# Kernel tuning notes

Measured on AMD Instinct MI355X. Metric: run time of the kernel, lower is better.

## Reference

```python
import jax, jax.numpy as jnp
import numpy as np

EPS = 1e-7
ROUTINGS = 3


def squash(s, axis=-1):
    # norm over `axis`; faithful to torch: (|s|^2/(1+|s|^2)) * (s/(|s|+eps))
    norm = jnp.linalg.norm(s, axis=axis, keepdims=True)
    sq = norm * norm
    return (sq / (1.0 + sq)) * (s / (norm + EPS))


def conv2d(x, w, b, stride):
    y = jax.lax.conv_general_dilated(
        x, w, window_strides=(stride, stride), padding='VALID',
        dimension_numbers=('NCHW', 'OIHW', 'NCHW'))
    return y + b[None, :, None, None]


def setup_inputs() -> dict:
    key = jax.random.key(0)
    ks = jax.random.split(key, 12)
    B = 256
    return {
        'x': jax.random.normal(ks[0], (B, 1, 28, 28), dtype=jnp.float32),
        'conv1_w': 0.05 * jax.random.normal(ks[1], (256, 1, 9, 9), dtype=jnp.float32),
        'conv1_b': jnp.zeros((256,), jnp.float32),
        'conv2_w': 0.02 * jax.random.normal(ks[2], (256, 256, 9, 9), dtype=jnp.float32),
        'conv2_b': jnp.zeros((256,), jnp.float32),
        'W_caps': 0.01 * jax.random.normal(ks[3], (10, 1152, 16, 8), dtype=jnp.float32),
        'dec_w1': 0.05 * jax.random.normal(ks[4], (160, 512), dtype=jnp.float32),
        'dec_b1': jnp.zeros((512,), jnp.float32),
        'dec_w2': 0.04 * jax.random.normal(ks[5], (512, 1024), dtype=jnp.float32),
        'dec_b2': jnp.zeros((1024,), jnp.float32),
        'dec_w3': 0.03 * jax.random.normal(ks[6], (1024, 784), dtype=jnp.float32),
        'dec_b3': jnp.zeros((784,), jnp.float32),
    }


def reference(x, conv1_w, conv1_b, conv2_w, conv2_b, W_caps,
              dec_w1, dec_b1, dec_w2, dec_b2, dec_w3, dec_b3):
    B = x.shape[0]
    # conv1: [B,1,28,28] -> [B,256,20,20]
    h = conv2d(x, conv1_w, conv1_b, stride=1)
    # primary capsules: conv -> [B,256,6,6]
    h = conv2d(h, conv2_w, conv2_b, stride=2)
    # faithful to original: squash over the LAST spatial axis (dim=-1)
    h = squash(h, axis=-1)
    u = h.reshape(B, -1, 8)  # [B,1152,8]

    # u_hat[b,o,i,d] = W_caps[o,i,d,e] @ u[b,i,e]  -> [B,10,1152,16]
    u_hat = jnp.einsum('oide,bie->boid', W_caps, u)
    u_hat_det = jax.lax.stop_gradient(u_hat)

    b_logits = jnp.zeros((B, 10, 1152), u_hat.dtype)
    for it in range(ROUTINGS):
        c = jax.nn.softmax(b_logits, axis=1)  # over output capsules
        if it == ROUTINGS - 1:
            v = squash(jnp.sum(c[:, :, :, None] * u_hat, axis=-2, keepdims=True))
        else:
            v = squash(jnp.sum(c[:, :, :, None] * u_hat_det, axis=-2, keepdims=True))
            b_logits = b_logits + jnp.sum(v * u_hat_det, axis=-1)
    v = jnp.squeeze(v, axis=-2)  # [B,10,16]

    length = jnp.linalg.norm(v, axis=-1)  # [B,10]
    # y defaults to one-hot of argmax(length), constant w.r.t. grads
    y = jax.lax.stop_gradient(
        jax.nn.one_hot(jnp.argmax(length, axis=1), 10, dtype=v.dtype))
    masked = (v * y[:, :, None]).reshape(B, -1)  # [B,160]
    h1 = jax.nn.relu(masked @ dec_w1 + dec_b1)
    h2 = jax.nn.relu(h1 @ dec_w2 + dec_b2)
    reconstruction = jax.nn.sigmoid(h2 @ dec_w3 + dec_b3)  # [B,784]
    return length, reconstruction
```

## Files before the change

### kernel.cpp

```cpp
#include <hip/hip_runtime.h>
#include <cstdint>
#include <cstddef>

typedef __bf16 bf16x8 __attribute__((ext_vector_type(8)));
typedef float  floatx4 __attribute__((ext_vector_type(4)));
typedef float  floatx2 __attribute__((ext_vector_type(2)));
typedef float  floatx16 __attribute__((ext_vector_type(16)));
typedef int    intx4v __attribute__((ext_vector_type(4)));
typedef int    intx8 __attribute__((ext_vector_type(8)));
typedef unsigned short ushort8 __attribute__((ext_vector_type(8)));
typedef unsigned short ushort4v __attribute__((ext_vector_type(4)));

__device__ __forceinline__ float bflo(unsigned int u) {
    union { unsigned int u32; float f; } x; x.u32 = u << 16; return x.f;
}
__device__ __forceinline__ float bfhi(unsigned int u) {
    union { unsigned int u32; float f; } x; x.u32 = u & 0xffff0000u; return x.f;
}
__device__ __forceinline__ unsigned short f2bf(float f) {
    union { float f; unsigned int u; } x; x.f = f;
    unsigned int u = x.u;
    unsigned int r = (u + 0x7fffu + ((u >> 16) & 1u)) >> 16;
    return (unsigned short)r;
}
__device__ __forceinline__ unsigned char f2fp8(float f) {
    unsigned int pk = __builtin_amdgcn_cvt_pk_fp8_f32(f, f, 0, false);
    return (unsigned char)(pk & 0xff);
}
__device__ __forceinline__ void fp8x4_dec(unsigned int u, float* f) {
    floatx2 lo = __builtin_amdgcn_cvt_pk_f32_fp8(u, false);
    floatx2 hi = __builtin_amdgcn_cvt_pk_f32_fp8(u, true);
    f[0] = lo[0]; f[1] = lo[1]; f[2] = hi[0]; f[3] = hi[1];
}

#define GLOBAL_U32 const __attribute__((address_space(1))) unsigned int*
#define LDS_U32 __attribute__((address_space(3))) unsigned int*
__device__ __forceinline__ void async_cp16(const void* g, void* l) {
    __builtin_amdgcn_global_load_lds((GLOBAL_U32)g, (LDS_U32)l, 16, 0, 0);
}

#define UHAT_SCALE 64.0f
#define UHAT_INV   (1.0f / 64.0f)
#define W2_SCALE   16.0f
#define W2_INV     (1.0f / 16.0f)

__global__ __launch_bounds__(256) void prep_k(const float* __restrict__ x,
                                              const float* __restrict__ w1c,
                                              const float* __restrict__ b1c,
                                              const float* __restrict__ w2,
                                              unsigned char* __restrict__ h1t8,
                                              unsigned char* __restrict__ w2t8,
                                              float* __restrict__ S012) {
    const int blk = blockIdx.x, t = threadIdx.x;
    if (t < 120) S012[blk * 120 + t] = 0.f;
    __shared__ float shm[10368];
    if (blk < 512) {
        const int b = blk >> 1, hh = blk & 1;
        const int oh0 = hh * 10;
        for (int idx = t; idx < 504; idx += 256) shm[idx] = x[b * 784 + oh0 * 28 + idx];
        __syncthreads();
        const float* wr = w1c + t * 81;
        const float bv = b1c[t];
        for (int ohl = 0; ohl < 10; ++ohl) {
            float acc[20];
#pragma unroll
            for (int ow = 0; ow < 20; ++ow) acc[ow] = bv;
#pragma unroll
            for (int kh = 0; kh < 9; ++kh) {
                float xr[28];
                const float* xrow = &shm[(ohl + kh) * 28];
#pragma unroll
                for (int q = 0; q < 7; ++q) *(float4*)&xr[q * 4] = *(const float4*)&xrow[q * 4];
#pragma unroll
                for (int kw = 0; kw < 9; ++kw) {
                    const float wv = wr[kh * 9 + kw];
#pragma unroll
                    for (int ow = 0; ow < 20; ++ow) acc[ow] = fmaf(xr[ow + kw], wv, acc[ow]);
                }
            }
            unsigned char* orow = h1t8 + (size_t)((b * 20 + oh0 + ohl) * 20) * 256 + t;
#pragma unroll
            for (int ow = 0; ow < 20; ++ow) orow[ow * 256] = f2fp8(acc[ow]);
        }
    } else {
        const int id = blk - 512;
        const int oc = id >> 1, half = id & 1;
        const float* src = w2 + (size_t)oc * 20736 + half * 128 * 81;
        for (int idx = t; idx < 10368; idx += 256) shm[idx] = src[idx];
        __syncthreads();
        unsigned char* dst = w2t8 + (size_t)oc * 20736 + half * 128;
        for (int idx = t; idx < 10368; idx += 256) {
            const int tap = idx >> 7, icl = idx & 127;
            dst[tap * 256 + icl] = f2fp8(shm[icl * 81 + tap] * W2_SCALE);
        }
    }
}

__device__ __forceinline__ int c2_rowbase(int m) {
    const int b = m / 36, sp = m % 36;
    const int oh = sp / 6, ow = sp % 6;
    return (b * 400 + oh * 40 + ow * 2) * 256;
}

__global__ __launch_bounds__(256) void conv2_k(const unsigned char* __restrict__ h1t8,
                                               const unsigned char* __restrict__ w2t8,
                                               unsigned short* __restrict__ part) {
    const int t = threadIdx.x;
    const int id = blockIdx.x;
    const int G = id >> 4;
    const int bx = (id >> 3) & 1;
    const int s = id & 7;
    const int by = 2 * G + (s >> 2);
    const int z  = ((s & 3) + by) & 3;
    __shared__ unsigned char At[128 * 128];
    __shared__ unsigned char Bt[128 * 128];

    const int oc0 = bx * 128;

    int aRB[4], bBase[4];
#pragma unroll
    for (int k = 0; k < 4; ++k) {
        const int a = t + 256 * k;
        const int r = a >> 3, sg = a & 7;
        const int u = sg ^ (r & 7);
        aRB[k] = c2_rowbase(by * 128 + r) + u * 16;
        bBase[k] = (oc0 + r) * 20736 + u * 16;
    }

    const int lane = t & 63, l31 = lane & 31, h = lane >> 5;
    const int wave = t >> 6;
    const int wM = (wave & 1) * 64, wOC = (wave >> 1) * 64;

    int aO[2][2][2], bO[2][2][2];
#pragma unroll
    for (int i = 0; i < 2; ++i) {
        const int Ra = wOC + i * 32 + l31;
        const int Rb = wM + i * 32 + l31;
#pragma unroll
        for (int st = 0; st < 2; ++st)
#pragma unroll
            for (int p = 0; p < 2; ++p) {
                const int c = st * 4 + h * 2 + p;
                aO[st][i][p] = Ra * 128 + ((c ^ (Ra & 7)) << 4);
                bO[st][i][p] = Rb * 128 + ((c ^ (Rb & 7)) << 4);
            }
    }

    floatx16 acc[2][2];
#pragma unroll
    for (int i = 0; i < 2; ++i)
#pragma unroll
        for (int j = 0; j < 2; ++j)
#pragma unroll
            for (int r = 0; r < 16; ++r) acc[i][j][r] = 0.f;

    const int q0 = (162 * z) >> 2, q1 = (162 * (z + 1)) >> 2;
    for (int q = q0; q < q1; ++q) {
        const int tap = q >> 1;
        const int kh = tap / 9, kw = tap - 9 * kh;
        const int aoffB = (kh * 20 + kw) * 256 + (q & 1) * 128;
        __syncthreads();
#pragma unroll
        for (int k = 0; k < 4; ++k)
            async_cp16(h1t8 + aRB[k] + aoffB, At + (t + 256 * k) * 16);
#pragma unroll
        for (int k = 0; k < 4; ++k)
            async_cp16(w2t8 + bBase[k] + q * 128, Bt + (t + 256 * k) * 16);
        __syncthreads();
#pragma unroll
        for (int st = 0; st < 2; ++st) {
            intx8 aF[2], bF[2];
#pragma unroll
            for (int i = 0; i < 2; ++i) {
                const intx4v alo = *(const intx4v*)(Bt + aO[st][i][0]);
                const intx4v ahi = *(const intx4v*)(Bt + aO[st][i][1]);
                aF[i] = (intx8){alo[0], alo[1], alo[2], alo[3], ahi[0], ahi[1], ahi[2], ahi[3]};
                const intx4v blo = *(const intx4v*)(At + bO[st][i][0]);
                const intx4v bhi = *(const intx4v*)(At + bO[st][i][1]);
                bF[i] = (intx8){blo[0], blo[1], blo[2], blo[3], bhi[0], bhi[1], bhi[2], bhi[3]};
            }
#pragma unroll
            for (int i = 0; i < 2; ++i)
#pragma unroll
                for (int j = 0; j < 2; ++j)
                    acc[i][j] = __builtin_amdgcn_mfma_scale_f32_32x32x64_f8f6f4(
                        aF[i], bF[j], acc[i][j], 0, 0, 0, 127, 0, 127);
        }
    }

    unsigned short* pz = part + (size_t)z * 2359296;
#pragma unroll
    for (int i = 0; i < 2; ++i) {
#pragma unroll
        for (int j = 0; j < 2; ++j) {
            const int m = by * 128 + wM + j * 32 + l31;
#pragma unroll
            for (int rg = 0; rg < 4; ++rg) {
                const int oc = oc0 + wOC + i * 32 + rg * 8 + 4 * h;
                ushort4v pk;
#pragma unroll
                for (int rr = 0; rr < 4; ++rr) pk[rr] = f2bf(acc[i][j][rg * 4 + rr] * W2_INV);
                *(ushort4v*)(pz + (size_t)m * 256 + oc) = pk;
            }
        }
    }
}

__global__ __launch_bounds__(256) void squash_u_k(const unsigned short* __restrict__ part,
                                                  const float* __restrict__ bias,
                                                  float* __restrict__ u) {
    const int bb = blockIdx.x, t = threadIdx.x;
    const int b = bb >> 1, h = bb & 1;
    __shared__ float hs[4608];
    const size_t base = (size_t)b * 9216 + h * 4608;
    for (int q = t; q < 2304; q += 256) {
        const int idx = q * 2;
        float v0 = bias[idx & 255], v1 = bias[(idx + 1) & 255];
#pragma unroll
        for (int z = 0; z < 4; ++z) {
            const unsigned int uu = *(const unsigned int*)(part + (size_t)z * 2359296 + base + idx);
            v0 += bflo(uu);
            v1 += bfhi(uu);
        }
        hs[idx] = v0; hs[idx + 1] = v1;
    }
    __syncthreads();
    for (int gq = t; gq < 768; gq += 256) {
        const int c = gq / 3, ohl = gq % 3;
        const int oh = h * 3 + ohl;
        float s[6], sq = 0.f;
#pragma unroll
        for (int ow = 0; ow < 6; ++ow) { s[ow] = hs[(ohl * 6 + ow) * 256 + c]; sq = fmaf(s[ow], s[ow], sq); }
        const float norm = sqrtf(sq);
        const float f = (sq / (1.0f + sq)) / (norm + 1e-7f);
        float* up = u + (size_t)b * 9216 + c * 36 + oh * 6;
#pragma unroll
        for (int ow = 0; ow < 6; ++ow) up[ow] = s[ow] * f;
    }
}

__global__ __launch_bounds__(256) void uhat_k(const float* __restrict__ Wc,
                                              const float* __restrict__ u,
                                              unsigned int* __restrict__ uhat8) {
    const int i = blockIdx.x, t = threadIdx.x;
    __shared__ float Wl[1280];
    for (int idx = t; idx < 1280; idx += 256) {
        const int o = idx >> 7, r = idx & 127;
        Wl[idx] = Wc[((size_t)o * 1152 + i) * 128 + r];
    }
    float ur[8];
    *(float4*)&ur[0] = *(const float4*)(u + (size_t)t * 9216 + i * 8);
    *(float4*)&ur[4] = *(const float4*)(u + (size_t)t * 9216 + i * 8 + 4);
    __syncthreads();
    unsigned int* row = uhat8 + ((size_t)i * 256 + t) * 40;
#pragma unroll 1
    for (int o = 0; o < 10; ++o) {
        float vals[16];
#pragma unroll
        for (int d = 0; d < 16; ++d) {
            const float* wp = &Wl[o * 128 + d * 8];
            float a = 0.f;
#pragma unroll
            for (int e = 0; e < 8; ++e) a = fmaf(wp[e], ur[e], a);
            vals[d] = a * UHAT_SCALE;
        }
        uint4 pk;
        unsigned int w;
#pragma unroll
        for (int q = 0; q < 4; ++q) {
            w = 0;
            w = __builtin_amdgcn_cvt_pk_fp8_f32(vals[q * 4 + 0], vals[q * 4 + 1], w, false);
            w = __builtin_amdgcn_cvt_pk_fp8_f32(vals[q * 4 + 2], vals[q * 4 + 3], w, true);
            if (q == 0) pk.x = w; else if (q == 1) pk.y = w; else if (q == 2) pk.z = w; else pk.w = w;
        }
        *(uint4*)(row + o * 4) = pk;
    }
}

__global__ __launch_bounds__(256) void route_iter0_k(const unsigned int* __restrict__ uhat8,
                                                     float* __restrict__ S0) {
    const int b = blockIdx.x, i0 = blockIdx.y * 128, t = threadIdx.x;
    const int th = t & 127, hi = t >> 7;
    if (th >= 40) return;
    const unsigned int* p = uhat8 + ((size_t)(i0 + hi * 64) * 256 + b) * 40 + th;
    float a0 = 0.f, a1 = 0.f, a2 = 0.f, a3 = 0.f;
#pragma unroll 4
    for (int i = 0; i < 64; ++i) {
        float f[4];
        fp8x4_dec(p[(size_t)i * 10240], f);
        a0 += f[0]; a1 += f[1]; a2 += f[2]; a3 += f[3];
    }
    const float sc = 0.1f * UHAT_INV;
    atomicAdd(&S0[b * 160 + 4 * th + 0], sc * a0);
    atomicAdd(&S0[b * 160 + 4 * th + 1], sc * a1);
    atomicAdd(&S0[b * 160 + 4 * th + 2], sc * a2);
    atomicAdd(&S0[b * 160 + 4 * th + 3], sc * a3);
}

template <int ITER>
__global__ __launch_bounds__(256) void route_iter_k(const unsigned int* __restrict__ uhat8,
                                                    const float* __restrict__ S_in,
                                                    float* __restrict__ BL,
                                                    float* __restrict__ S_out) {
    const int b = blockIdx.x, i0 = blockIdx.y * 128, t = threadIdx.x;
    __shared__ __align__(16) unsigned int Ul8[128 * 40];
    __shared__ float Vl[160];
    __shared__ float cT[10 * 132];
    __shared__ float dots[128 * 10];

    const unsigned int* ub = uhat8 + ((size_t)i0 * 256 + b) * 40;
#pragma unroll
    for (int rep = 0; rep < 5; ++rep) {
        const int c = rep * 256 + t;
        const int row = c / 10, q = c - row * 10;
        async_cp16(ub + (size_t)row * 10240 + q * 4, (char*)Ul8 + c * 16);
    }

    if (t < 160) {
        const float x = S_in[b * 160 + t];
        float sq = x * x;
        sq += __shfl_xor(sq, 1, 16);
        sq += __shfl_xor(sq, 2, 16);
        sq += __shfl_xor(sq, 4, 16);
        sq += __shfl_xor(sq, 8, 16);
        const float norm = sqrtf(sq);
        const float f = (sq / (1.f + sq)) / (norm + 1e-7f);
        Vl[t] = x * f;
    }
    __syncthreads();

    const int o = t % 10, s = t / 10;
    float vr[16];
    if (t < 250) {
#pragma unroll
        for (int q = 0; q < 4; ++q)
            *(float4*)&vr[q * 4] = *(const float4*)(&Vl[o * 16 + q * 4]);
    }

    if (t < 250) {
#pragma unroll
        for (int rep = 0; rep < 6; ++rep) {
            const int i = s + 25 * rep;
            if (i < 128) {
                const uint4 uu = *(const uint4*)(Ul8 + i * 40 + o * 4);
                float f[16];
                fp8x4_dec(uu.x, f);
                fp8x4_dec(uu.y, f + 4);
                fp8x4_dec(uu.z, f + 8);
                fp8x4_dec(uu.w, f + 12);
                float dot = 0.f;
#pragma unroll
                for (int d = 0; d < 16; ++d) dot = fmaf(f[d], vr[d], dot);
                dots[i * 10 + o] = dot * UHAT_INV;
            }
        }
    }
    __syncthreads();

    if (t < 128) {
        float bl[10];
#pragma unroll
        for (int oo = 0; oo < 10; ++oo) bl[oo] = dots[t * 10 + oo];
        if (ITER == 2) {
#pragma unroll
            for (int oo = 0; oo < 10; ++oo) bl[oo] += BL[(size_t)b * 11520 + oo * 1152 + i0 + t];
        } else {
#pragma unroll
            for (int oo = 0; oo < 10; ++oo) BL[(size_t)b * 11520 + oo * 1152 + i0 + t] = bl[oo];
        }
        float mx = bl[0];
#pragma unroll
        for (int oo = 1; oo < 10; ++oo) mx = fmaxf(mx, bl[oo]);
        float ex[10], sum = 0.f;
#pragma unroll
        for (int oo = 0; oo < 10; ++oo) { ex[oo] = expf(bl[oo] - mx); sum += ex[oo]; }
        const float inv = 1.f / sum;
#pragma unroll
        for (int oo = 0; oo < 10; ++oo) cT[oo * 132 + t] = ex[oo] * inv;
    }
    __syncthreads();

    const int th = t & 127, hi = t >> 7;
    if (th < 40) {
        const int oq = th >> 2;
        const unsigned int* base = Ul8 + hi * 64 * 40 + th;
        const float* cb = &cT[oq * 132 + hi * 64];
        float a0 = 0.f, a1 = 0.f, a2 = 0.f, a3 = 0.f;
#pragma unroll 4
        for (int ii = 0; ii < 64; ++ii) {
            const float c = cb[ii];
            float f[4];
            fp8x4_dec(base[ii * 40], f);
            a0 = fmaf(c, f[0], a0);
            a1 = fmaf(c, f[1], a1);
            a2 = fmaf(c, f[2], a2);
            a3 = fmaf(c, f[3], a3);
        }
        atomicAdd(&S_out[b * 160 + 4 * th + 0], a0 * UHAT_INV);
        atomicAdd(&S_out[b * 160 + 4 * th + 1], a1 * UHAT_INV);
        atomicAdd(&S_out[b * 160 + 4 * th + 2], a2 * UHAT_INV);
        atomicAdd(&S_out[b * 160 + 4 * th + 3], a3 * UHAT_INV);
    }
}

__global__ __launch_bounds__(512) void final_k(const float* __restrict__ S,
                                               const float* __restrict__ w1,
                                               const float* __restrict__ b1,
                                               float* __restrict__ out_len,
                                               float* __restrict__ h1d) {
    const int b = blockIdx.x, t = threadIdx.x;
    __shared__ float v_s[160];
    __shared__ float len_s[10];
    __shared__ int sel_s;
    if (t < 160) {
        const float x = S[b * 160 + t];
        float sq = x * x;
        sq += __shfl_xor(sq, 1, 16);
        sq += __shfl_xor(sq, 2, 16);
        sq += __shfl_xor(sq, 4, 16);
        sq += __shfl_xor(sq, 8, 16);
        const float norm = sqrtf(sq);
        const float f = (sq / (1.f + sq)) / (norm + 1e-7f);
        v_s[t] = x * f;
        if ((t & 15) == 0) {
            const float len = f * norm;
            len_s[t >> 4] = len;
            out_len[b * 10 + (t >> 4)] = len;
        }
    }
    __syncthreads();
    if (t == 0) {
        float best = len_s[0]; int bi = 0;
        for (int oo = 1; oo < 10; ++oo) if (len_s[oo] > best) { best = len_s[oo]; bi = oo; }
        sel_s = bi;
    }
    __syncthreads();
    const int s = sel_s;
    float acc = b1[t];
    const float* wrow = w1 + (size_t)(s * 16) * 512 + t;
#pragma unroll
    for (int j = 0; j < 16; ++j) acc = fmaf(v_s[s * 16 + j], wrow[j * 512], acc);
    h1d[(size_t)b * 512 + t] = fmaxf(acc, 0.f);
}

template <int ACT>
__global__ __launch_bounds__(256) void mlp3_k(const float* __restrict__ A,
                                              const float* __restrict__ Bm,
                                              const float* __restrict__ bias,
                                              float* __restrict__ C, int N, int K) {
    extern __shared__ float Asm[];
    const int t = threadIdx.x;
    const int m0 = blockIdx.y * 8, n0 = blockIdx.x * 64;
    const int RS = K + 4;
    const int k4 = K >> 2;
    for (int i = t; i < 8 * k4; i += 256) {
        const int r = i / k4, c = i - r * k4;
        *(float4*)&Asm[r * RS + c * 4] = *(const float4*)&A[(size_t)(m0 + r) * K + c * 4];
    }
    __syncthreads();
    const int lane = t & 63, w = t >> 6;
    const int mq = lane >> 4, nq = lane & 15;
    const int n = n0 + nq * 4;
    const int ncl = (n + 3 < N) ? n : (N - 4);
    const float* bp = Bm + ncl;
    const float* asA = &Asm[(mq * 2 + 0) * RS];
    const float* asB = &Asm[(mq * 2 + 1) * RS];
    const int kQ = K >> 2;
    const int kBeg = w * kQ;
    const int nBat2 = kQ >> 4;
    float4 acc0 = {0.f, 0.f, 0.f, 0.f}, acc1 = {0.f, 0.f, 0.f, 0.f};
    float4 ba[8], bb[8];
#pragma unroll
    for (int d = 0; d < 8; ++d) ba[d] = *(const float4*)&bp[(size_t)(kBeg + d) * N];

#define MLP3_FMA(BATCH, KB)                                                       \
    _Pragma("unroll")                                                             \
    for (int d = 0; d < 8; ++d) {                                                 \
        const float4 b = BATCH[d];                                                \
        const float a0 = asA[(KB) + d];                                           \
        const float a1 = asB[(KB) + d];                                           \
        acc0.x = fmaf(a0, b.x, acc0.x); acc0.y = fmaf(a0, b.y, acc0.y);           \
        acc0.z = fmaf(a0, b.z, acc0.z); acc0.w = fmaf(a0, b.w, acc0.w);           \
        acc1.x = fmaf(a1, b.x, acc1.x); acc1.y = fmaf(a1, b.y, acc1.y);           \
        acc1.z = fmaf(a1, b.z, acc1.z); acc1.w = fmaf(a1, b.w, acc1.w);           \
    }

    int k = kBeg;
#pragma unroll 1
    for (int it = 0; it < nBat2; ++it) {
#pragma unroll
        for (int d = 0; d < 8; ++d) bb[d] = *(const float4*)&bp[(size_t)(k + 8 + d) * N];
        MLP3_FMA(ba, k)
        if (it + 1 < nBat2) {
#pragma unroll
            for (int d = 0; d < 8; ++d) ba[d] = *(const float4*)&bp[(size_t)(k + 16 + d) * N];
        }
        MLP3_FMA(bb, k + 8)
        k += 16;
    }
#undef MLP3_FMA

    __syncthreads();
    float* red = Asm;
    float* my = &red[(size_t)(w * 64 + lane) * 8];
    my[0] = acc0.x; my[1] = acc0.y; my[2] = acc0.z; my[3] = acc0.w;
    my[4] = acc1.x; my[5] = acc1.y; my[6] = acc1.z; my[7] = acc1.w;
    __syncthreads();
    if (t < 64) {
        float o[8];
#pragma unroll
        for (int x = 0; x < 8; ++x)
            o[x] = red[(size_t)t * 8 + x] + red[(size_t)(64 + t) * 8 + x]
                 + red[(size_t)(128 + t) * 8 + x] + red[(size_t)(192 + t) * 8 + x];
        const int nn = n0 + (t & 15) * 4;
#pragma unroll
        for (int rm = 0; rm < 2; ++rm) {
            const int m = m0 + (t >> 4) * 2 + rm;
#pragma unroll
            for (int rn = 0; rn < 4; ++rn) {
                const int ncol = nn + rn;
                if (ncol < N) {
                    float v = o[rm * 4 + rn] + bias[ncol];
                    if (ACT == 0) v = fmaxf(v, 0.f);
                    else v = 1.f / (1.f + expf(-v));
                    C[(size_t)m * N + ncol] = v;
                }
            }
        }
    }
}

extern "C" void kernel_launch(void* const* d_in, const int* in_sizes, int n_in,
                              void* d_out, int out_size, void* d_ws, size_t ws_size,
                              hipStream_t stream) {
    const float* x   = (const float*)d_in[0];
    const float* w1  = (const float*)d_in[1];
    const float* b1  = (const float*)d_in[2];
    const float* w2  = (const float*)d_in[3];
    const float* b2  = (const float*)d_in[4];
    const float* Wc  = (const float*)d_in[5];
    const float* dw1 = (const float*)d_in[6];
    const float* db1 = (const float*)d_in[7];
    const float* dw2 = (const float*)d_in[8];
    const float* db2 = (const float*)d_in[9];
    const float* dw3 = (const float*)d_in[10];
    const float* db3 = (const float*)d_in[11];
    float* out = (float*)d_out;

    char* ws = (char*)d_ws;
    unsigned char* H1T8 = (unsigned char*)(ws + 0);
    unsigned char* W2T8 = (unsigned char*)(ws + 26214400);
    unsigned short* PART = (unsigned short*)(ws + 31522816);
    unsigned int*   UHAT = (unsigned int*)(ws + 0);
    float* U    = (float*)(ws + 50397184);
    float* BL   = (float*)(ws + 59834368);
    float* S012 = (float*)(ws + 71630848);
    float* H1D  = (float*)(ws + 59834368);
    float* H2D  = (float*)(ws + 60358656);

    float* S0 = S012, *S1 = S012 + 40960, *S2 = S012 + 81920;

    prep_k<<<1024, 256, 0, stream>>>(x, w1, b1, w2, H1T8, W2T8, S012);
    conv2_k<<<576, 256, 0, stream>>>(H1T8, W2T8, PART);
    squash_u_k<<<512, 256, 0, stream>>>(PART, b2, U);
    uhat_k<<<1152, 256, 0, stream>>>(Wc, U, UHAT);
    route_iter0_k<<<dim3(256, 9), 256, 0, stream>>>(UHAT, S0);
    route_iter_k<1><<<dim3(256, 9), 256, 0, stream>>>(UHAT, S0, BL, S1);
    route_iter_k<2><<<dim3(256, 9), 256, 0, stream>>>(UHAT, S1, BL, S2);
    final_k<<<256, 512, 0, stream>>>(S2, dw1, db1, out, H1D);
    mlp3_k<0><<<dim3(16, 32), 256, 8 * 516 * 4, stream>>>(H1D, dw2, db2, H2D, 1024, 512);
    mlp3_k<1><<<dim3(13, 32), 256, 8 * 1028 * 4, stream>>>(H2D, dw3, db3, out + 2560, 784, 1024);
}
```

Measured before the change: 345.5 us.

## Widen conv2 tile to all 256 channels, split-K by 8, finer conv1 blocks

conv2 blocks now cover all 256 output channels at once, so each A (activation) tile is loaded once rather than twice. To keep the grid at 576 blocks, the reduction is split into 8 parts instead of 4, and the launch bound asks for two blocks per CU. conv1 is split into quarter-height blocks to give more parallelism, and the workspace layout is reshuffled so the larger partial buffer fits. The cost is twice as much bf16 partial-sum traffic to write and then sum in squash, more accumulator registers per thread, and 48KB of LDS per block.

After: 374.8 us. 1.08x slower.

```diff
diff --git a/kernel.cpp b/kernel.cpp
--- a/kernel.cpp
+++ b/kernel.cpp
@@ -52,16 +52,16 @@
                                               unsigned char* __restrict__ w2t8,
                                               float* __restrict__ S012) {
     const int blk = blockIdx.x, t = threadIdx.x;
-    if (t < 120) S012[blk * 120 + t] = 0.f;
+    if (t < 80) S012[blk * 80 + t] = 0.f;
     __shared__ float shm[10368];
-    if (blk < 512) {
-        const int b = blk >> 1, hh = blk & 1;
-        const int oh0 = hh * 10;
-        for (int idx = t; idx < 504; idx += 256) shm[idx] = x[b * 784 + oh0 * 28 + idx];
+    if (blk < 1024) {
+        const int b = blk >> 2, hh = blk & 3;
+        const int oh0 = hh * 5;
+        for (int idx = t; idx < 364; idx += 256) shm[idx] = x[b * 784 + oh0 * 28 + idx];
         __syncthreads();
         const float* wr = w1c + t * 81;
         const float bv = b1c[t];
-        for (int ohl = 0; ohl < 10; ++ohl) {
+        for (int ohl = 0; ohl < 5; ++ohl) {
             float acc[20];
 #pragma unroll
             for (int ow = 0; ow < 20; ++ow) acc[ow] = bv;
@@ -83,7 +83,7 @@
             for (int ow = 0; ow < 20; ++ow) orow[ow * 256] = f2fp8(acc[ow]);
         }
     } else {
-        const int id = blk - 512;
+        const int id = blk - 1024;
         const int oc = id >> 1, half = id & 1;
         const float* src = w2 + (size_t)oc * 20736 + half * 128 * 81;
         for (int idx = t; idx < 10368; idx += 256) shm[idx] = src[idx];
@@ -102,59 +102,69 @@
     return (b * 400 + oh * 40 + ow * 2) * 256;
 }
 
-__global__ __launch_bounds__(256) void conv2_k(const unsigned char* __restrict__ h1t8,
-                                               const unsigned char* __restrict__ w2t8,
-                                               unsigned short* __restrict__ part) {
+__global__ __launch_bounds__(256, 2) void conv2_k(const unsigned char* __restrict__ h1t8,
+                                                  const unsigned char* __restrict__ w2t8,
+                                                  unsigned short* __restrict__ part) {
     const int t = threadIdx.x;
     const int id = blockIdx.x;
-    const int G = id >> 4;
-    const int bx = (id >> 3) & 1;
-    const int s = id & 7;
-    const int by = 2 * G + (s >> 2);
-    const int z  = ((s & 3) + by) & 3;
+    const int by = id >> 3;
+    const int z  = id & 7;
     __shared__ unsigned char At[128 * 128];
-    __shared__ unsigned char Bt[128 * 128];
-
-    const int oc0 = bx * 128;
-
-    int aRB[4], bBase[4];
+    __shared__ unsigned char Bt[256 * 128];
+
+    int aRB[4], bBase[8];
 #pragma unroll
     for (int k = 0; k < 4; ++k) {
         const int a = t + 256 * k;
         const int r = a >> 3, sg = a & 7;
         const int u = sg ^ (r & 7);
         aRB[k] = c2_rowbase(by * 128 + r) + u * 16;
-        bBase[k] = (oc0 + r) * 20736 + u * 16;
+    }
+#pragma unroll
+    for (int k = 0; k < 8; ++k) {
+        const int a = t + 256 * k;
+        const int r = a >> 3, sg = a & 7;
+        const int u = sg ^ (r & 7);
+        bBase[k] = r * 20736 + u * 16;
     }
 
     const int lane = t & 63, l31 = lane & 31, h = lane >> 5;
     const int wave = t >> 6;
-    const int wM = (wave & 1) * 64, wOC = (wave >> 1) * 64;
-
-    int aO[2][2][2], bO[2][2][2];
-#pragma unroll
-    for (int i = 0; i < 2; ++i) {
+    const int wM = (wave & 1) * 64, wOC = (wave >> 1) * 128;
+
+    int aO[2][4][2], bO[2][2][2];
+#pragma unroll
+    for (int i = 0; i < 4; ++i) {
         const int Ra = wOC + i * 32 + l31;
-        const int Rb = wM + i * 32 + l31;
 #pragma unroll
         for (int st = 0; st < 2; ++st)
 #pragma unroll
             for (int p = 0; p < 2; ++p) {
                 const int c = st * 4 + h * 2 + p;
                 aO[st][i][p] = Ra * 128 + ((c ^ (Ra & 7)) << 4);
-                bO[st][i][p] = Rb * 128 + ((c ^ (Rb & 7)) << 4);
-            }
-    }
-
-    floatx16 acc[2][2];
-#pragma unroll
-    for (int i = 0; i < 2; ++i)
+            }
+    }
+#pragma unroll
+    for (int j = 0; j < 2; ++j) {
+        const int Rb = wM + j * 32 + l31;
+#pragma unroll
+        for (int st = 0; st < 2; ++st)
+#pragma unroll
+            for (int p = 0; p < 2; ++p) {
+                const int c = st * 4 + h * 2 + p;
+                bO[st][j][p] = Rb * 128 + ((c ^ (Rb & 7)) << 4);
+            }
+    }
+
+    floatx16 acc[4][2];
+#pragma unroll
+    for (int i = 0; i < 4; ++i)
 #pragma unroll
         for (int j = 0; j < 2; ++j)
 #pragma unroll
             for (int r = 0; r < 16; ++r) acc[i][j][r] = 0.f;
 
-    const int q0 = (162 * z) >> 2, q1 = (162 * (z + 1)) >> 2;
+    const int q0 = (162 * z) >> 3, q1 = (162 * (z + 1)) >> 3;
     for (int q = q0; q < q1; ++q) {
         const int tap = q >> 1;
         const int kh = tap / 9, kw = tap - 9 * kh;
@@ -164,23 +174,26 @@
         for (int k = 0; k < 4; ++k)
             async_cp16(h1t8 + aRB[k] + aoffB, At + (t + 256 * k) * 16);
 #pragma unroll
-        for (int k = 0; k < 4; ++k)
+        for (int k = 0; k < 8; ++k)
             async_cp16(w2t8 + bBase[k] + q * 128, Bt + (t + 256 * k) * 16);
         __syncthreads();
 #pragma unroll
         for (int st = 0; st < 2; ++st) {
-            intx8 aF[2], bF[2];
-#pragma unroll
-            for (int i = 0; i < 2; ++i) {
+            intx8 aF[4], bF[2];
+#pragma unroll
+            for (int i = 0; i < 4; ++i) {
                 const intx4v alo = *(const intx4v*)(Bt + aO[st][i][0]);
                 const intx4v ahi = *(const intx4v*)(Bt + aO[st][i][1]);
                 aF[i] = (intx8){alo[0], alo[1], alo[2], alo[3], ahi[0], ahi[1], ahi[2], ahi[3]};
-                const intx4v blo = *(const intx4v*)(At + bO[st][i][0]);
-                const intx4v bhi = *(const intx4v*)(At + bO[st][i][1]);
-                bF[i] = (intx8){blo[0], blo[1], blo[2], blo[3], bhi[0], bhi[1], bhi[2], bhi[3]};
-            }
-#pragma unroll
-            for (int i = 0; i < 2; ++i)
+            }
+#pragma unroll
+            for (int j = 0; j < 2; ++j) {
+                const intx4v blo = *(const intx4v*)(At + bO[st][j][0]);
+                const intx4v bhi = *(const intx4v*)(At + bO[st][j][1]);
+                bF[j] = (intx8){blo[0], blo[1], blo[2], blo[3], bhi[0], bhi[1], bhi[2], bhi[3]};
+            }
+#pragma unroll
+            for (int i = 0; i < 4; ++i)
 #pragma unroll
                 for (int j = 0; j < 2; ++j)
                     acc[i][j] = __builtin_amdgcn_mfma_scale_f32_32x32x64_f8f6f4(
@@ -190,13 +203,13 @@
 
     unsigned short* pz = part + (size_t)z * 2359296;
 #pragma unroll
-    for (int i = 0; i < 2; ++i) {
+    for (int i = 0; i < 4; ++i) {
 #pragma unroll
         for (int j = 0; j < 2; ++j) {
             const int m = by * 128 + wM + j * 32 + l31;
 #pragma unroll
             for (int rg = 0; rg < 4; ++rg) {
-                const int oc = oc0 + wOC + i * 32 + rg * 8 + 4 * h;
+                const int oc = wOC + i * 32 + rg * 8 + 4 * h;
                 ushort4v pk;
 #pragma unroll
                 for (int rr = 0; rr < 4; ++rr) pk[rr] = f2bf(acc[i][j][rg * 4 + rr] * W2_INV);
@@ -217,7 +230,7 @@
         const int idx = q * 2;
         float v0 = bias[idx & 255], v1 = bias[(idx + 1) & 255];
 #pragma unroll
-        for (int z = 0; z < 4; ++z) {
+        for (int z = 0; z < 8; ++z) {
             const unsigned int uu = *(const unsigned int*)(part + (size_t)z * 2359296 + base + idx);
             v0 += bflo(uu);
             v1 += bfhi(uu);
@@ -551,16 +564,16 @@
     unsigned char* H1T8 = (unsigned char*)(ws + 0);
     unsigned char* W2T8 = (unsigned char*)(ws + 26214400);
     unsigned short* PART = (unsigned short*)(ws + 31522816);
-    unsigned int*   UHAT = (unsigned int*)(ws + 0);
-    float* U    = (float*)(ws + 50397184);
-    float* BL   = (float*)(ws + 59834368);
+    float* U    = (float*)(ws + 0);
+    unsigned int* UHAT = (unsigned int*)(ws + 9437184);
+    float* BL   = (float*)(ws + 56623104);
     float* S012 = (float*)(ws + 71630848);
-    float* H1D  = (float*)(ws + 59834368);
-    float* H2D  = (float*)(ws + 60358656);
+    float* H1D  = (float*)(ws + 68419584);
+    float* H2D  = (float*)(ws + 68943872);
 
     float* S0 = S012, *S1 = S012 + 40960, *S2 = S012 + 81920;
 
-    prep_k<<<1024, 256, 0, stream>>>(x, w1, b1, w2, H1T8, W2T8, S012);
+    prep_k<<<1536, 256, 0, stream>>>(x, w1, b1, w2, H1T8, W2T8, S012);
     conv2_k<<<576, 256, 0, stream>>>(H1T8, W2T8, PART);
     squash_u_k<<<512, 256, 0, stream>>>(PART, b2, U);
     uhat_k<<<1152, 256, 0, stream>>>(Wc, U, UHAT);
```

## Load conv2 MFMA fragments straight from global and split conv1 across more blocks

Applied to the files above, without the earlier changes.

conv2_k no longer stages A and B tiles through LDS with async copies and two barriers per K step. Each lane now loads its 16-byte fp8 fragments directly from global memory into registers, and the kernel requests 3 blocks per CU through launch bounds. This removes LDS traffic and synchronisation, but waves that share rows now read them redundantly, relying on L1/L2 instead of shared memory. Separately, prep_k splits conv1 into 4 row-chunks per image instead of 2, giving 1024 conv1 blocks for more parallelism, and the zeroing of S012 is re-strided to match the new grid.

After: 518.1 us. +50.0%, slower.

```diff
diff --git a/kernel.cpp b/kernel.cpp
--- a/kernel.cpp
+++ b/kernel.cpp
@@ -52,16 +52,16 @@
                                               unsigned char* __restrict__ w2t8,
                                               float* __restrict__ S012) {
     const int blk = blockIdx.x, t = threadIdx.x;
-    if (t < 120) S012[blk * 120 + t] = 0.f;
+    if (t < 80) S012[blk * 80 + t] = 0.f;
     __shared__ float shm[10368];
-    if (blk < 512) {
-        const int b = blk >> 1, hh = blk & 1;
-        const int oh0 = hh * 10;
-        for (int idx = t; idx < 504; idx += 256) shm[idx] = x[b * 784 + oh0 * 28 + idx];
+    if (blk < 1024) {
+        const int b = blk >> 2, hh = blk & 3;
+        const int oh0 = hh * 5;
+        for (int idx = t; idx < 364; idx += 256) shm[idx] = x[b * 784 + oh0 * 28 + idx];
         __syncthreads();
         const float* wr = w1c + t * 81;
         const float bv = b1c[t];
-        for (int ohl = 0; ohl < 10; ++ohl) {
+        for (int ohl = 0; ohl < 5; ++ohl) {
             float acc[20];
 #pragma unroll
             for (int ow = 0; ow < 20; ++ow) acc[ow] = bv;
@@ -83,7 +83,7 @@
             for (int ow = 0; ow < 20; ++ow) orow[ow * 256] = f2fp8(acc[ow]);
         }
     } else {
-        const int id = blk - 512;
+        const int id = blk - 1024;
         const int oc = id >> 1, half = id & 1;
         const float* src = w2 + (size_t)oc * 20736 + half * 128 * 81;
         for (int idx = t; idx < 10368; idx += 256) shm[idx] = src[idx];
@@ -102,9 +102,9 @@
     return (b * 400 + oh * 40 + ow * 2) * 256;
 }
 
-__global__ __launch_bounds__(256) void conv2_k(const unsigned char* __restrict__ h1t8,
-                                               const unsigned char* __restrict__ w2t8,
-                                               unsigned short* __restrict__ part) {
+__global__ __launch_bounds__(256, 3) void conv2_k(const unsigned char* __restrict__ h1t8,
+                                                  const unsigned char* __restrict__ w2t8,
+                                                  unsigned short* __restrict__ part) {
     const int t = threadIdx.x;
     const int id = blockIdx.x;
     const int G = id >> 4;
@@ -112,39 +112,16 @@
     const int s = id & 7;
     const int by = 2 * G + (s >> 2);
     const int z  = ((s & 3) + by) & 3;
-    __shared__ unsigned char At[128 * 128];
-    __shared__ unsigned char Bt[128 * 128];
-
     const int oc0 = bx * 128;
-
-    int aRB[4], bBase[4];
-#pragma unroll
-    for (int k = 0; k < 4; ++k) {
-        const int a = t + 256 * k;
-        const int r = a >> 3, sg = a & 7;
-        const int u = sg ^ (r & 7);
-        aRB[k] = c2_rowbase(by * 128 + r) + u * 16;
-        bBase[k] = (oc0 + r) * 20736 + u * 16;
-    }
 
     const int lane = t & 63, l31 = lane & 31, h = lane >> 5;
     const int wave = t >> 6;
     const int wM = (wave & 1) * 64, wOC = (wave >> 1) * 64;
 
-    int aO[2][2][2], bO[2][2][2];
-#pragma unroll
-    for (int i = 0; i < 2; ++i) {
-        const int Ra = wOC + i * 32 + l31;
-        const int Rb = wM + i * 32 + l31;
-#pragma unroll
-        for (int st = 0; st < 2; ++st)
-#pragma unroll
-            for (int p = 0; p < 2; ++p) {
-                const int c = st * 4 + h * 2 + p;
-                aO[st][i][p] = Ra * 128 + ((c ^ (Ra & 7)) << 4);
-                bO[st][i][p] = Rb * 128 + ((c ^ (Rb & 7)) << 4);
-            }
-    }
+    const unsigned char* aRow0 = w2t8 + (size_t)(oc0 + wOC + l31) * 20736 + h * 32;
+    const unsigned char* aRow1 = w2t8 + (size_t)(oc0 + wOC + 32 + l31) * 20736 + h * 32;
+    const unsigned char* bRow0 = h1t8 + c2_rowbase(by * 128 + wM + l31) + h * 32;
+    const unsigned char* bRow1 = h1t8 + c2_rowbase(by * 128 + wM + 32 + l31) + h * 32;
 
     floatx16 acc[2][2];
 #pragma unroll
@@ -158,26 +135,28 @@
     for (int q = q0; q < q1; ++q) {
         const int tap = q >> 1;
         const int kh = tap / 9, kw = tap - 9 * kh;
-        const int aoffB = (kh * 20 + kw) * 256 + (q & 1) * 128;
-        __syncthreads();
-#pragma unroll
-        for (int k = 0; k < 4; ++k)
-            async_cp16(h1t8 + aRB[k] + aoffB, At + (t + 256 * k) * 16);
-#pragma unroll
-        for (int k = 0; k < 4; ++k)
-            async_cp16(w2t8 + bBase[k] + q * 128, Bt + (t + 256 * k) * 16);
-        __syncthreads();
+        const int offB = (kh * 20 + kw) * 256 + (q & 1) * 128;
+        const int offA = q * 128;
+        intx4v av[2][2][2], bv[2][2][2];
+#pragma unroll
+        for (int st = 0; st < 2; ++st)
+#pragma unroll
+            for (int p = 0; p < 2; ++p) {
+                const int d = st * 64 + p * 16;
+                av[0][st][p] = *(const intx4v*)(aRow0 + offA + d);
+                av[1][st][p] = *(const intx4v*)(aRow1 + offA + d);
+                bv[0][st][p] = *(const intx4v*)(bRow0 + offB + d);
+                bv[1][st][p] = *(const intx4v*)(bRow1 + offB + d);
+            }
 #pragma unroll
         for (int st = 0; st < 2; ++st) {
             intx8 aF[2], bF[2];
 #pragma unroll
             for (int i = 0; i < 2; ++i) {
-                const intx4v alo = *(const intx4v*)(Bt + aO[st][i][0]);
-                const intx4v ahi = *(const intx4v*)(Bt + aO[st][i][1]);
-                aF[i] = (intx8){alo[0], alo[1], alo[2], alo[3], ahi[0], ahi[1], ahi[2], ahi[3]};
-                const intx4v blo = *(const intx4v*)(At + bO[st][i][0]);
-                const intx4v bhi = *(const intx4v*)(At + bO[st][i][1]);
-                bF[i] = (intx8){blo[0], blo[1], blo[2], blo[3], bhi[0], bhi[1], bhi[2], bhi[3]};
+                aF[i] = (intx8){av[i][st][0][0], av[i][st][0][1], av[i][st][0][2], av[i][st][0][3],
+                                av[i][st][1][0], av[i][st][1][1], av[i][st][1][2], av[i][st][1][3]};
+                bF[i] = (intx8){bv[i][st][0][0], bv[i][st][0][1], bv[i][st][0][2], bv[i][st][0][3],
+                                bv[i][st][1][0], bv[i][st][1][1], bv[i][st][1][2], bv[i][st][1][3]};
             }
 #pragma unroll
             for (int i = 0; i < 2; ++i)
@@ -560,7 +539,7 @@
 
     float* S0 = S012, *S1 = S012 + 40960, *S2 = S012 + 81920;
 
-    prep_k<<<1024, 256, 0, stream>>>(x, w1, b1, w2, H1T8, W2T8, S012);
+    prep_k<<<1536, 256, 0, stream>>>(x, w1, b1, w2, H1T8, W2T8, S012);
     conv2_k<<<576, 256, 0, stream>>>(H1T8, W2T8, PART);
     squash_u_k<<<512, 256, 0, stream>>>(PART, b2, U);
     uhat_k<<<1152, 256, 0, stream>>>(Wc, U, UHAT);
```
